# Optimization experiments

Hardware: AMD Instinct MI355X
Metric: run time of the kernel (lower is better)

The kernel has to match this reference:

```python
import jax, jax.numpy as jnp
import numpy as np

D_MODEL, N_HEAD, D_FFN = 1024, 16, 4096
MAX_REL = 128
NUM_BUCKETS = 2 * MAX_REL - 1  # 255
B, T = 2, 2048


def algebraic_ln(x, gamma, beta, a, b_raw, eps=1e-5):
    mean = jnp.mean(x, axis=-1, keepdims=True)
    var = jnp.var(x, axis=-1, keepdims=True)  # unbiased=False
    z = var + eps
    b = jax.nn.softplus(10.0 * b_raw) / 10.0  # softplus with beta=10
    p = a[0] + a[1] * z + a[2] * z ** 2
    q = b[0] + b[1] * z + b[2] * z ** 2
    return (x - mean) * (p / q) * gamma + beta


def setup_inputs() -> dict:
    key = jax.random.key(0)
    ks = jax.random.split(key, 16)
    s = (1.0 / np.sqrt(D_MODEL)).astype(np.float32)
    inp = {
        'x': jax.random.normal(ks[0], (B, T, D_MODEL), jnp.float32),
        'casual_mask': jnp.tril(jnp.ones((T, T), dtype=bool)),
        'Wq': jax.random.normal(ks[1], (D_MODEL, D_MODEL), jnp.float32) * s,
        'bq': jnp.zeros((D_MODEL,), jnp.float32),
        'Wk': jax.random.normal(ks[2], (D_MODEL, D_MODEL), jnp.float32) * s,
        'bk': jnp.zeros((D_MODEL,), jnp.float32),
        'Wv': jax.random.normal(ks[3], (D_MODEL, D_MODEL), jnp.float32) * s,
        'bv': jnp.zeros((D_MODEL,), jnp.float32),
        'Wo': jax.random.normal(ks[4], (D_MODEL, D_MODEL), jnp.float32) * s,
        'bo': jnp.zeros((D_MODEL,), jnp.float32),
        'rel_emb': jax.random.normal(ks[5], (NUM_BUCKETS, N_HEAD), jnp.float32) * 0.02,
        'g1': jnp.ones((D_MODEL,), jnp.float32),
        'be1': jnp.zeros((D_MODEL,), jnp.float32),
        'a1': jnp.array([1.0, 0.5, 0.1], jnp.float32),
        'br1': jnp.array([1.0, 0.3, 0.05], jnp.float32),
        'g2': jnp.ones((D_MODEL,), jnp.float32),
        'be2': jnp.zeros((D_MODEL,), jnp.float32),
        'a2': jnp.array([1.0, 0.5, 0.1], jnp.float32),
        'br2': jnp.array([1.0, 0.3, 0.05], jnp.float32),
        'W1': jax.random.normal(ks[6], (D_FFN, D_MODEL), jnp.float32) * s,
        'b1': jnp.zeros((D_FFN,), jnp.float32),
        'W2': jax.random.normal(ks[7], (D_MODEL, D_FFN), jnp.float32) * (1.0 / np.sqrt(D_FFN)),
        'b2': jnp.zeros((D_MODEL,), jnp.float32),
        'res_scale': jnp.array(0.5, jnp.float32),
    }
    return inp


def attention(x, mask, Wq, bq, Wk, bk, Wv, bv, Wo, bo, rel_emb):
    Bx, Tx, C = x.shape
    H, Dh = N_HEAD, C // N_HEAD
    scale = Dh ** -0.5
    Q = (x @ Wq.T + bq).reshape(Bx, Tx, H, Dh)
    K = (x @ Wk.T + bk).reshape(Bx, Tx, H, Dh)
    V = (x @ Wv.T + bv).reshape(Bx, Tx, H, Dh)
    scores = jnp.einsum('bqhd,bkhd->bhqk', Q, K) * scale
    rel = jnp.arange(Tx)[None, :] - jnp.arange(Tx)[:, None]  # k_pos - q_pos
    buckets = jnp.clip(rel, -MAX_REL + 1, MAX_REL - 1) + (MAX_REL - 1)
    bias = rel_emb[buckets]  # [T,T,H]
    scores = scores + jnp.transpose(bias, (2, 0, 1))[None]
    m = mask[None, None]  # [1,1,T,T]
    # torch: masked_fill(-inf) then masked_fill(0) -> masked entries become 0
    scores = jnp.where(m, scores, 0.0)
    w = jax.nn.relu(scores) + 1e-6
    w = jnp.where(m, w, 0.0)
    w = w / (jnp.sum(w, axis=-1, keepdims=True) + 1e-6)
    out = jnp.einsum('bhqk,bkhd->bqhd', w, V).reshape(Bx, Tx, C)
    return out @ Wo.T + bo


def reference(x, casual_mask, Wq, bq, Wk, bk, Wv, bv, Wo, bo, rel_emb,
              g1, be1, a1, br1, g2, be2, a2, br2, W1, b1, W2, b2, res_scale):
    scale = jnp.clip(res_scale, 0.2, 1.0)
    x = x + scale * attention(algebraic_ln(x, g1, be1, a1, br1), casual_mask,
                              Wq, bq, Wk, bk, Wv, bv, Wo, bo, rel_emb)
    h = algebraic_ln(x, g2, be2, a2, br2)
    ffn = jax.nn.relu(h @ W1.T + b1) @ W2.T + b2  # dropout is identity at eval
    return x + scale * ffn
```

## Files before the change

kernel.cpp:

```cpp
#include <hip/hip_runtime.h>
#include <stdint.h>


#define D_MODEL 1024
#define T_SEQ   2048
#define NHEAD   16
#define DH      64
#define DFFN    4096
#define MROWS   4096

using short8  = __attribute__((ext_vector_type(8))) short;
using floatx4 = __attribute__((ext_vector_type(4))) float;

__device__ __forceinline__ float bf2f(ushort u) {
    union { uint32_t i; float f; } x; x.i = ((uint32_t)u) << 16; return x.f;
}
__device__ __forceinline__ ushort f2bf(float f) {
    union { float f; uint32_t i; } x; x.f = f;
    uint32_t i = x.i;
    return (ushort)((i + 0x7fffu + ((i >> 16) & 1u)) >> 16);
}
__device__ __forceinline__ float ldf(const void* p, size_t i, int dt) {
    return dt ? bf2f(((const ushort*)p)[i]) : ((const float*)p)[i];
}
__device__ __forceinline__ int detect_bf16(const void* g1) {
    return *(const uint32_t*)g1 == 0x3F803F80u;
}
__device__ __forceinline__ void gld_lds16(const void* g, void* l) {
    __builtin_amdgcn_global_load_lds(
        (__attribute__((address_space(1))) uint32_t*)(g),
        (__attribute__((address_space(3))) uint32_t*)(l), 16, 0, 0);
}
__device__ __forceinline__ float softplus10(float t) {
    float u = 10.f * t;
    return (u > 20.f ? u : log1pf(expf(u))) * 0.1f;
}

template <int INMODE>
__global__ __launch_bounds__(256)
void ln_kernel(const void* __restrict__ xin,
               const void* __restrict__ gamma, const void* __restrict__ beta,
               const void* __restrict__ a3, const void* __restrict__ br3,
               ushort* __restrict__ out, const void* __restrict__ dtprobe)
{
    const int dt = detect_bf16(dtprobe);
    const int row = blockIdx.x;
    const int tid = threadIdx.x;
    const int col = tid * 4;
    float v[4];
    if (INMODE == 1) {
        const float* x = (const float*)xin + (size_t)row * D_MODEL;
        float4 t = *(const float4*)(x + col);
        v[0] = t.x; v[1] = t.y; v[2] = t.z; v[3] = t.w;
    } else if (dt) {
        const ushort* x = (const ushort*)xin + (size_t)row * D_MODEL;
        ushort4 t = *(const ushort4*)(x + col);
        v[0] = bf2f(t.x); v[1] = bf2f(t.y); v[2] = bf2f(t.z); v[3] = bf2f(t.w);
    } else {
        const float* x = (const float*)xin + (size_t)row * D_MODEL;
        float4 t = *(const float4*)(x + col);
        v[0] = t.x; v[1] = t.y; v[2] = t.z; v[3] = t.w;
    }
    float s  = v[0] + v[1] + v[2] + v[3];
    float s2 = v[0]*v[0] + v[1]*v[1] + v[2]*v[2] + v[3]*v[3];
#pragma unroll
    for (int m = 32; m > 0; m >>= 1) {
        s  += __shfl_down(s,  m, 64);
        s2 += __shfl_down(s2, m, 64);
    }
    __shared__ float wsum[4], wsum2[4];
    const int wave = tid >> 6, lane = tid & 63;
    if (lane == 0) { wsum[wave] = s; wsum2[wave] = s2; }
    __syncthreads();
    s  = wsum[0] + wsum[1] + wsum[2] + wsum[3];
    s2 = wsum2[0] + wsum2[1] + wsum2[2] + wsum2[3];
    const float mean = s * (1.f / D_MODEL);
    const float var  = s2 * (1.f / D_MODEL) - mean * mean;
    const float z = var + 1e-5f;
    const float a0 = ldf(a3, 0, dt), a1 = ldf(a3, 1, dt), a2 = ldf(a3, 2, dt);
    const float b0 = softplus10(ldf(br3, 0, dt));
    const float b1 = softplus10(ldf(br3, 1, dt));
    const float b2 = softplus10(ldf(br3, 2, dt));
    const float p = a0 + a1 * z + a2 * z * z;
    const float q = b0 + b1 * z + b2 * z * z;
    const float f = p / q;
    ushort4 o; ushort* op = (ushort*)&o;
#pragma unroll
    for (int e = 0; e < 4; e++) {
        op[e] = f2bf((v[e] - mean) * f * ldf(gamma, col + e, dt) + ldf(beta, col + e, dt));
    }
    *(ushort4*)(out + (size_t)row * D_MODEL + col) = o;
}

template <int MODE, int BM, int BN>
__global__ __launch_bounds__(256)
void gemm_bt(const ushort* __restrict__ A,
             const void* __restrict__ Bw0, const void* __restrict__ Bw1,
             const void* __restrict__ Bw2,
             const void* __restrict__ bias0, const void* __restrict__ bias1,
             const void* __restrict__ bias2,
             void* __restrict__ C0, void* __restrict__ C1, void* __restrict__ C2v,
             int Nst, int K, const void* __restrict__ dtprobe)
{
    constexpr int NI = BM / 32;
    constexpr int NJ = BN / 32;
    constexpr int AC = BM / 64;
    constexpr int BC = BN / 64;
    __shared__ __align__(16) ushort As[BM * 32];
    __shared__ __align__(16) ushort Bs[BN * 32];
    const int dt = detect_bf16(dtprobe);
    const int tid  = threadIdx.x;
    const int wave = tid >> 6, lane = tid & 63;
    const int wr = wave >> 1, wc = wave & 1;
    const int g = lane >> 4, l15 = lane & 15;

    const void* Bw = Bw0; const void* bias = bias0; void* Cout = C0;
    if (MODE == 4) {
        const int mat = blockIdx.x >> 3;
        if (mat == 1)      { Bw = Bw1; bias = bias1; Cout = C1; }
        else if (mat == 2) { Bw = Bw2; bias = bias2; Cout = C2v; }
    }
    const int m0 = blockIdx.y * BM;
    const int n0 = (MODE == 4) ? ((blockIdx.x & 7) * 128) : (blockIdx.x * BN);

    floatx4 acc[NI][NJ];
#pragma unroll
    for (int i = 0; i < NI; i++)
#pragma unroll
        for (int j = 0; j < NJ; j++) acc[i][j] = {0.f, 0.f, 0.f, 0.f};

    const int srow = lane >> 2;
    const int ssw  = (srow >> 1) & 3;
    const int scol = (((lane & 3) ^ ssw) * 8);
    const int fsw  = (l15 >> 1) & 3;
    for (int k0 = 0; k0 < K; k0 += 32) {
        __syncthreads();
        if (dt) {
            const ushort* Bb = (const ushort*)Bw;
#pragma unroll
            for (int c = 0; c < AC; c++) {
                const int r0 = (wave * AC + c) * 16;
                gld_lds16(A + (size_t)(m0 + r0 + srow) * K + k0 + scol, &As[r0 * 32]);
            }
#pragma unroll
            for (int c = 0; c < BC; c++) {
                const int r0 = (wave * BC + c) * 16;
                gld_lds16(Bb + (size_t)(n0 + r0 + srow) * K + k0 + scol, &Bs[r0 * 32]);
            }
        } else {
            const float* Bf = (const float*)Bw;
#pragma unroll
            for (int c = 0; c < AC; c++) {
                const int r0 = (wave * AC + c) * 16;
                gld_lds16(A + (size_t)(m0 + r0 + srow) * K + k0 + scol, &As[r0 * 32]);
            }
#pragma unroll
            for (int c = 0; c < BC; c++) {
                const int r0 = (wave * BC + c) * 16;
                const float* src = Bf + (size_t)(n0 + r0 + srow) * K + k0 + scol;
                float4 t0 = *(const float4*)(src);
                float4 t1 = *(const float4*)(src + 4);
                ushort tmp[8] = { f2bf(t0.x), f2bf(t0.y), f2bf(t0.z), f2bf(t0.w),
                                  f2bf(t1.x), f2bf(t1.y), f2bf(t1.z), f2bf(t1.w) };
                *(short8*)&Bs[(r0 + srow) * 32 + (lane & 3) * 8] = *(short8*)tmp;
            }
        }
        __syncthreads();
        short8 af[NI], bfr[NJ];
#pragma unroll
        for (int i = 0; i < NI; i++)
            af[i]  = *(const short8*)&As[(wr * (BM / 2) + i * 16 + l15) * 32 + ((g ^ fsw) * 8)];
#pragma unroll
        for (int j = 0; j < NJ; j++)
            bfr[j] = *(const short8*)&Bs[(wc * (BN / 2) + j * 16 + l15) * 32 + ((g ^ fsw) * 8)];
#pragma unroll
        for (int i = 0; i < NI; i++)
#pragma unroll
            for (int j = 0; j < NJ; j++)
                acc[i][j] = __builtin_amdgcn_mfma_f32_16x16x32_bf16(af[i], bfr[j], acc[i][j], 0, 0, 0);
    }

#pragma unroll
    for (int i = 0; i < NI; i++) {
        const int rowb = m0 + wr * (BM / 2) + i * 16 + g * 4;
#pragma unroll
        for (int j = 0; j < NJ; j++) {
            const int col = n0 + wc * (BN / 2) + j * 16 + l15;
            const float bi = ldf(bias, col, dt);
#pragma unroll
            for (int r = 0; r < 4; r++) {
                const size_t idx = (size_t)(rowb + r) * Nst + col;
                const float v = acc[i][j][r] + bi;
                if (MODE == 1) ((ushort*)Cout)[idx] = f2bf(fmaxf(v, 0.f));
                else           ((ushort*)Cout)[idx] = f2bf(v);
            }
        }
    }
}

template <int MODE>
__global__ __launch_bounds__(256)
void gemm_k64p(const ushort* __restrict__ A, const void* __restrict__ Bw,
               const void* __restrict__ bias, void* __restrict__ Cout,
               const void* __restrict__ resid, const void* __restrict__ scale_p,
               int Nst, int K, const void* __restrict__ dtprobe)
{
    __shared__ __align__(16) ushort As[2][2][64 * 32];
    __shared__ __align__(16) ushort Bs[2][2][64 * 32];
    const int dt = detect_bf16(dtprobe);
    const int tid  = threadIdx.x;
    const int wave = tid >> 6, lane = tid & 63;
    const int wr = wave >> 1, wc = wave & 1;
    const int g = lane >> 4, l15 = lane & 15;
    const int m0 = blockIdx.y * 64, n0 = blockIdx.x * 64;

    floatx4 acc[2][2];
#pragma unroll
    for (int i = 0; i < 2; i++)
#pragma unroll
        for (int j = 0; j < 2; j++) acc[i][j] = {0.f, 0.f, 0.f, 0.f};

    const int srow = lane >> 2;
    const int ssw  = (srow >> 1) & 3;
    const int scol = (((lane & 3) ^ ssw) * 8);
    const int fsw  = (l15 >> 1) & 3;
    const int r0   = wave * 16;

    auto stage = [&](int buf, int k0) {
        if (dt) {
            const ushort* Bb = (const ushort*)Bw;
#pragma unroll
            for (int kb = 0; kb < 2; kb++) {
                gld_lds16(A  + (size_t)(m0 + r0 + srow) * K + k0 + kb * 32 + scol, &As[buf][kb][r0 * 32]);
                gld_lds16(Bb + (size_t)(n0 + r0 + srow) * K + k0 + kb * 32 + scol, &Bs[buf][kb][r0 * 32]);
            }
        } else {
            const float* Bf = (const float*)Bw;
#pragma unroll
            for (int kb = 0; kb < 2; kb++) {
                gld_lds16(A + (size_t)(m0 + r0 + srow) * K + k0 + kb * 32 + scol, &As[buf][kb][r0 * 32]);
                const float* src = Bf + (size_t)(n0 + r0 + srow) * K + k0 + kb * 32 + scol;
                float4 t0 = *(const float4*)(src);
                float4 t1 = *(const float4*)(src + 4);
                ushort tmp[8] = { f2bf(t0.x), f2bf(t0.y), f2bf(t0.z), f2bf(t0.w),
                                  f2bf(t1.x), f2bf(t1.y), f2bf(t1.z), f2bf(t1.w) };
                *(short8*)&Bs[buf][kb][(r0 + srow) * 32 + (lane & 3) * 8] = *(short8*)tmp;
            }
        }
    };

    const int nt = K >> 6;
    stage(0, 0);
    __syncthreads();
    int cur = 0;
    for (int t = 0; t < nt; ++t) {
        if (t + 1 < nt) stage(cur ^ 1, (t + 1) << 6);
        short8 af[2][2], bfr[2][2];
#pragma unroll
        for (int kb = 0; kb < 2; kb++) {
#pragma unroll
            for (int i = 0; i < 2; i++)
                af[i][kb]  = *(const short8*)&As[cur][kb][(wr * 32 + i * 16 + l15) * 32 + ((g ^ fsw) * 8)];
#pragma unroll
            for (int j = 0; j < 2; j++)
                bfr[j][kb] = *(const short8*)&Bs[cur][kb][(wc * 32 + j * 16 + l15) * 32 + ((g ^ fsw) * 8)];
        }
#pragma unroll
        for (int kb = 0; kb < 2; kb++)
#pragma unroll
            for (int i = 0; i < 2; i++)
#pragma unroll
                for (int j = 0; j < 2; j++)
                    acc[i][j] = __builtin_amdgcn_mfma_f32_16x16x32_bf16(af[i][kb], bfr[j][kb], acc[i][j], 0, 0, 0);
        __syncthreads();
        cur ^= 1;
    }

    const float scl = fminf(fmaxf(ldf(scale_p, 0, dt), 0.2f), 1.0f);
#pragma unroll
    for (int i = 0; i < 2; i++) {
        const int rowb = m0 + wr * 32 + i * 16 + g * 4;
#pragma unroll
        for (int j = 0; j < 2; j++) {
            const int col = n0 + wc * 32 + j * 16 + l15;
            const float bi = ldf(bias, col, dt);
#pragma unroll
            for (int r = 0; r < 4; r++) {
                const size_t idx = (size_t)(rowb + r) * Nst + col;
                const float v = acc[i][j][r] + bi;
                if (MODE == 2) ((float*)Cout)[idx] = ldf(resid, idx, dt) + scl * v;
                else {
                    const float o = ((const float*)resid)[idx] + scl * v;
                    if (dt) ((ushort*)Cout)[idx] = f2bf(o);
                    else    ((float*)Cout)[idx]  = o;
                }
            }
        }
    }
}

__global__ __launch_bounds__(256)
void attn_kernel(const ushort* __restrict__ Q, const ushort* __restrict__ K,
                 const ushort* __restrict__ V, const void* __restrict__ rel,
                 ushort* __restrict__ Out, const void* __restrict__ dtprobe)
{
    __shared__ __align__(16) ushort Ks[64 * 64];
    __shared__ __align__(16) ushort Vt[64 * 88];
    __shared__ __align__(16) ushort Ss[64 * 88];
    __shared__ float rel_h[128];
    __shared__ float den_l[64];

    const int dt = detect_bf16(dtprobe);
    const int tid  = threadIdx.x;
    const int wave = tid >> 6, lane = tid & 63;
    const int wr = wave >> 1, wc = wave & 1;
    const int g = lane >> 4, l15 = lane & 15;
    const int pair = blockIdx.x, h = blockIdx.y, b = blockIdx.z;

    if (tid < 128) rel_h[tid] = ldf(rel, (size_t)tid * NHEAD + h, dt);
    const float scale = 0.125f;

    for (int ph = 0; ph < 2; ph++) {
        const int qt = ph ? (31 - pair) : pair;
        __syncthreads();
        if (tid < 64) den_l[tid] = 0.f;

        const ushort* Qg = Q + ((size_t)(b * T_SEQ + qt * 64)) * D_MODEL + h * DH;
        short8 qa[2][2];
#pragma unroll
        for (int i = 0; i < 2; i++)
#pragma unroll
            for (int ks = 0; ks < 2; ks++)
                qa[i][ks] = *(const short8*)(Qg + (size_t)(wr * 32 + i * 16 + l15) * D_MODEL
                                             + (ks * 4 + g) * 8);

        floatx4 onum[2][2];
#pragma unroll
        for (int i = 0; i < 2; i++) { onum[i][0] = {0.f,0.f,0.f,0.f}; onum[i][1] = {0.f,0.f,0.f,0.f}; }
        float den_p[2][4];
#pragma unroll
        for (int i = 0; i < 2; i++)
#pragma unroll
            for (int r = 0; r < 4; r++) den_p[i][r] = 0.f;

        const int nk = qt + 1;
        for (int kt = 0; kt < nk; kt++) {
            const int kbase = kt * 64;
            __syncthreads();
            const ushort* Kg = K + ((size_t)(b * T_SEQ + kbase)) * D_MODEL + h * DH;
            {
                const int lrow = lane >> 3, pch = lane & 7;
#pragma unroll
                for (int c = 0; c < 2; c++) {
                    const int r0 = (wave * 2 + c) * 8;
                    const int row = r0 + lrow;
                    gld_lds16(Kg + (size_t)row * D_MODEL + ((pch ^ (row & 7)) * 8), &Ks[r0 * 64]);
                }
            }
            const ushort* Vg = V + ((size_t)(b * T_SEQ + kbase)) * D_MODEL + h * DH;
#pragma unroll
            for (int c = 0; c < 2; c++) {
                const int chunk = tid + c * 256;
                const int krow = chunk >> 3;
                const int bb   = chunk & 7;
                short8 t = *(const short8*)(Vg + (size_t)krow * D_MODEL + bb * 8);
                ushort tmp[8]; *(short8*)tmp = t;
#pragma unroll
                for (int e = 0; e < 8; e++) {
                    const int ee = (e + bb) & 7;
                    Vt[(bb * 8 + ee) * 88 + krow] = tmp[ee];
                }
            }
            __syncthreads();

            floatx4 sacc[2][2];
#pragma unroll
            for (int i = 0; i < 2; i++) { sacc[i][0] = {0.f,0.f,0.f,0.f}; sacc[i][1] = {0.f,0.f,0.f,0.f}; }
#pragma unroll
            for (int ks = 0; ks < 2; ks++) {
                short8 kb[2];
                const int ch = ks * 4 + g;
#pragma unroll
                for (int j = 0; j < 2; j++) {
                    const int row = wc * 32 + j * 16 + l15;
                    kb[j] = *(const short8*)&Ks[row * 64 + ((ch ^ (row & 7)) * 8)];
                }
#pragma unroll
                for (int i = 0; i < 2; i++)
#pragma unroll
                    for (int j = 0; j < 2; j++)
                        sacc[i][j] = __builtin_amdgcn_mfma_f32_16x16x32_bf16(qa[i][ks], kb[j], sacc[i][j], 0, 0, 0);
            }

            const int dq = qt - kt;
            if (dq >= 3) {
                const float c0 = rel_h[0];
#pragma unroll
                for (int i = 0; i < 2; i++) {
                    const int qrow = wr * 32 + i * 16 + g * 4;
#pragma unroll
                    for (int j = 0; j < 2; j++) {
                        const int kcol = wc * 32 + j * 16 + l15;
#pragma unroll
                        for (int r = 0; r < 4; r++) {
                            const float w = fmaxf(sacc[i][j][r] * scale + c0, 0.f) + 1e-6f;
                            den_p[i][r] += w;
                            Ss[(qrow + r) * 88 + kcol] = f2bf(w);
                        }
                    }
                }
            } else {
#pragma unroll
                for (int i = 0; i < 2; i++) {
                    const int qrow = wr * 32 + i * 16 + g * 4;
#pragma unroll
                    for (int j = 0; j < 2; j++) {
                        const int kcol = wc * 32 + j * 16 + l15;
                        const int kg = kbase + kcol;
#pragma unroll
                        for (int r = 0; r < 4; r++) {
                            const int qg = qt * 64 + qrow + r;
                            const int d = qg - kg;
                            float w = 0.f;
                            if (d >= 0) {
                                const int bucket = 127 - (d < 127 ? d : 127);
                                const float sv = sacc[i][j][r] * scale + rel_h[bucket];
                                w = fmaxf(sv, 0.f) + 1e-6f;
                            }
                            den_p[i][r] += w;
                            Ss[(qrow + r) * 88 + kcol] = f2bf(w);
                        }
                    }
                }
            }
            __syncthreads();

#pragma unroll
            for (int ks = 0; ks < 2; ks++) {
                short8 wa[2], vb[2];
#pragma unroll
                for (int i = 0; i < 2; i++)
                    wa[i] = *(const short8*)&Ss[(wr * 32 + i * 16 + l15) * 88 + ks * 32 + g * 8];
#pragma unroll
                for (int j = 0; j < 2; j++)
                    vb[j] = *(const short8*)&Vt[(wc * 32 + j * 16 + l15) * 88 + ks * 32 + g * 8];
#pragma unroll
                for (int i = 0; i < 2; i++)
#pragma unroll
                    for (int j = 0; j < 2; j++)
                        onum[i][j] = __builtin_amdgcn_mfma_f32_16x16x32_bf16(wa[i], vb[j], onum[i][j], 0, 0, 0);
            }
        }

#pragma unroll
        for (int i = 0; i < 2; i++)
#pragma unroll
            for (int r = 0; r < 4; r++) {
                float v = den_p[i][r];
                v += __shfl_xor(v, 1, 64);
                v += __shfl_xor(v, 2, 64);
                v += __shfl_xor(v, 4, 64);
                v += __shfl_xor(v, 8, 64);
                den_p[i][r] = v;
            }
        __syncthreads();
        if (l15 == 0) {
#pragma unroll
            for (int i = 0; i < 2; i++)
#pragma unroll
                for (int r = 0; r < 4; r++)
                    atomicAdd(&den_l[wr * 32 + i * 16 + g * 4 + r], den_p[i][r]);
        }
        __syncthreads();

        const size_t obase = ((size_t)(b * T_SEQ + qt * 64)) * D_MODEL + h * DH;
#pragma unroll
        for (int i = 0; i < 2; i++) {
            const int qrow = wr * 32 + i * 16 + g * 4;
#pragma unroll
            for (int j = 0; j < 2; j++) {
                const int dcol = wc * 32 + j * 16 + l15;
#pragma unroll
                for (int r = 0; r < 4; r++) {
                    const float dn = den_l[qrow + r] + 1e-6f;
                    Out[obase + (size_t)(qrow + r) * D_MODEL + dcol] = f2bf(onum[i][j][r] / dn);
                }
            }
        }
    }
}

extern "C" void kernel_launch(void* const* d_in, const int* in_sizes, int n_in,
                              void* d_out, int out_size, void* d_ws, size_t ws_size,
                              hipStream_t stream)
{
    const void* x   = d_in[0];
    const void* Wq  = d_in[2];
    const void* bq  = d_in[3];
    const void* Wk  = d_in[4];
    const void* bk  = d_in[5];
    const void* Wv  = d_in[6];
    const void* bv  = d_in[7];
    const void* Wo  = d_in[8];
    const void* bo  = d_in[9];
    const void* rel = d_in[10];
    const void* g1  = d_in[11];
    const void* be1 = d_in[12];
    const void* a1  = d_in[13];
    const void* br1 = d_in[14];
    const void* g2  = d_in[15];
    const void* be2 = d_in[16];
    const void* a2  = d_in[17];
    const void* br2 = d_in[18];
    const void* W1  = d_in[19];
    const void* b1  = d_in[20];
    const void* W2  = d_in[21];
    const void* b2  = d_in[22];
    const void* rs  = d_in[23];

    char* ws = (char*)d_ws;
    ushort* ln1  = (ushort*)(ws);
    ushort* Qb   = (ushort*)(ws + (8u  << 20));
    ushort* Kb   = (ushort*)(ws + (16u << 20));
    ushort* Vb   = (ushort*)(ws + (24u << 20));
    ushort* atb  = (ushort*)(ws + (32u << 20));
    float*  x1   = (float*)(ws + (40u << 20));
    ushort* hbuf = (ushort*)(ws + (56u << 20));
    ushort* ffn1 = (ushort*)(ws);

    const dim3 blk(256);

    ln_kernel<0><<<dim3(MROWS), blk, 0, stream>>>(x, g1, be1, a1, br1, ln1, g1);
    gemm_bt<4, 128, 128><<<dim3(24, MROWS / 128), blk, 0, stream>>>(
        ln1, Wq, Wk, Wv, bq, bk, bv, Qb, Kb, Vb, D_MODEL, D_MODEL, g1);
    attn_kernel<<<dim3(16, NHEAD, 2), blk, 0, stream>>>(Qb, Kb, Vb, rel, atb, g1);
    gemm_k64p<2><<<dim3(D_MODEL / 64, MROWS / 64), blk, 0, stream>>>(
        atb, Wo, bo, x1, x, rs, D_MODEL, D_MODEL, g1);
    ln_kernel<1><<<dim3(MROWS), blk, 0, stream>>>(x1, g2, be2, a2, br2, hbuf, g1);
    gemm_bt<1, 128, 128><<<dim3(DFFN / 128, MROWS / 128), blk, 0, stream>>>(
        hbuf, W1, nullptr, nullptr, b1, nullptr, nullptr, ffn1, nullptr, nullptr,
        DFFN, D_MODEL, g1);
    gemm_k64p<3><<<dim3(D_MODEL / 64, MROWS / 64), blk, 0, stream>>>(
        ffn1, W2, b2, d_out, x1, rs, D_MODEL, DFFN, g1);
}
```

Baseline: 505.8 us.

## Split-K the FFN down-projection with atomic accumulation into the residual buffer

The final W2 GEMM (K=4096) is replaced by a split-K kernel over two K halves. Each half atomically adds its scaled partial sums into x1, which the second LN kernel has already pre-loaded with the residual plus scaled b2 bias. A separate cast kernel then writes the output in the input dtype. This doubles the number of blocks for the long-K GEMM to improve occupancy, at the cost of float atomics, non-deterministic summation order, and an extra pass over the output.

```diff
diff --git a/kernel.cpp b/kernel.cpp
--- a/kernel.cpp
+++ b/kernel.cpp
@@ -41,14 +41,15 @@
 void ln_kernel(const void* __restrict__ xin,
                const void* __restrict__ gamma, const void* __restrict__ beta,
                const void* __restrict__ a3, const void* __restrict__ br3,
-               ushort* __restrict__ out, const void* __restrict__ dtprobe)
+               ushort* __restrict__ out, const void* __restrict__ dtprobe,
+               const void* __restrict__ b2fold, const void* __restrict__ scale_p)
 {
     const int dt = detect_bf16(dtprobe);
     const int row = blockIdx.x;
     const int tid = threadIdx.x;
     const int col = tid * 4;
     float v[4];
-    if (INMODE == 1) {
+    if (INMODE >= 1) {
         const float* x = (const float*)xin + (size_t)row * D_MODEL;
         float4 t = *(const float4*)(x + col);
         v[0] = t.x; v[1] = t.y; v[2] = t.z; v[3] = t.w;
@@ -90,6 +91,33 @@
         op[e] = f2bf((v[e] - mean) * f * ldf(gamma, col + e, dt) + ldf(beta, col + e, dt));
     }
     *(ushort4*)(out + (size_t)row * D_MODEL + col) = o;
+    if (INMODE == 2) {
+        const float scl = fminf(fmaxf(ldf(scale_p, 0, dt), 0.2f), 1.0f);
+        float* xw = (float*)xin + (size_t)row * D_MODEL;
+        float4 t;
+        t.x = v[0] + scl * ldf(b2fold, col + 0, dt);
+        t.y = v[1] + scl * ldf(b2fold, col + 1, dt);
+        t.z = v[2] + scl * ldf(b2fold, col + 2, dt);
+        t.w = v[3] + scl * ldf(b2fold, col + 3, dt);
+        *(float4*)(xw + col) = t;
+    }
+}
+
+__global__ __launch_bounds__(256)
+void cast_out(const float* __restrict__ x1, void* __restrict__ out,
+              const void* __restrict__ dtprobe)
+{
+    const int dt = detect_bf16(dtprobe);
+    const int row = blockIdx.x;
+    const int col = threadIdx.x * 4;
+    float4 t = *(const float4*)(x1 + (size_t)row * D_MODEL + col);
+    if (dt) {
+        ushort4 o;
+        o.x = f2bf(t.x); o.y = f2bf(t.y); o.z = f2bf(t.z); o.w = f2bf(t.w);
+        *(ushort4*)((ushort*)out + (size_t)row * D_MODEL + col) = o;
+    } else {
+        *(float4*)((float*)out + (size_t)row * D_MODEL + col) = t;
+    }
 }
 
 template <int MODE, int BM, int BN>
@@ -294,6 +322,91 @@
                     if (dt) ((ushort*)Cout)[idx] = f2bf(o);
                     else    ((float*)Cout)[idx]  = o;
                 }
+            }
+        }
+    }
+}
+
+__global__ __launch_bounds__(256)
+void gemm_k64s(const ushort* __restrict__ A, const void* __restrict__ Bw,
+               float* __restrict__ Cacc, const void* __restrict__ scale_p,
+               int Nst, int K, int kext, const void* __restrict__ dtprobe)
+{
+    __shared__ __align__(16) ushort As[2][64 * 32];
+    __shared__ __align__(16) ushort Bs[2][64 * 32];
+    const int dt = detect_bf16(dtprobe);
+    const int tid  = threadIdx.x;
+    const int wave = tid >> 6, lane = tid & 63;
+    const int wr = wave >> 1, wc = wave & 1;
+    const int g = lane >> 4, l15 = lane & 15;
+    const int m0 = blockIdx.y * 64, n0 = blockIdx.x * 64;
+    const int ks0 = blockIdx.z * kext;
+
+    floatx4 acc[2][2];
+#pragma unroll
+    for (int i = 0; i < 2; i++)
+#pragma unroll
+        for (int j = 0; j < 2; j++) acc[i][j] = {0.f, 0.f, 0.f, 0.f};
+
+    const int srow = lane >> 2;
+    const int ssw  = (srow >> 1) & 3;
+    const int scol = (((lane & 3) ^ ssw) * 8);
+    const int fsw  = (l15 >> 1) & 3;
+    const int r0   = wave * 16;
+
+    for (int k0 = ks0; k0 < ks0 + kext; k0 += 64) {
+        __syncthreads();
+        if (dt) {
+            const ushort* Bb = (const ushort*)Bw;
+#pragma unroll
+            for (int kb = 0; kb < 2; kb++) {
+                gld_lds16(A  + (size_t)(m0 + r0 + srow) * K + k0 + kb * 32 + scol, &As[kb][r0 * 32]);
+                gld_lds16(Bb + (size_t)(n0 + r0 + srow) * K + k0 + kb * 32 + scol, &Bs[kb][r0 * 32]);
+            }
+        } else {
+            const float* Bf = (const float*)Bw;
+#pragma unroll
+            for (int kb = 0; kb < 2; kb++) {
+                gld_lds16(A + (size_t)(m0 + r0 + srow) * K + k0 + kb * 32 + scol, &As[kb][r0 * 32]);
+                const float* src = Bf + (size_t)(n0 + r0 + srow) * K + k0 + kb * 32 + scol;
+                float4 t0 = *(const float4*)(src);
+                float4 t1 = *(const float4*)(src + 4);
+                ushort tmp[8] = { f2bf(t0.x), f2bf(t0.y), f2bf(t0.z), f2bf(t0.w),
+                                  f2bf(t1.x), f2bf(t1.y), f2bf(t1.z), f2bf(t1.w) };
+                *(short8*)&Bs[kb][(r0 + srow) * 32 + (lane & 3) * 8] = *(short8*)tmp;
+            }
+        }
+        __syncthreads();
+        short8 af[2][2], bfr[2][2];
+#pragma unroll
+        for (int kb = 0; kb < 2; kb++) {
+#pragma unroll
+            for (int i = 0; i < 2; i++)
+                af[i][kb]  = *(const short8*)&As[kb][(wr * 32 + i * 16 + l15) * 32 + ((g ^ fsw) * 8)];
+#pragma unroll
+            for (int j = 0; j < 2; j++)
+                bfr[j][kb] = *(const short8*)&Bs[kb][(wc * 32 + j * 16 + l15) * 32 + ((g ^ fsw) * 8)];
+        }
+#pragma unroll
+        for (int kb = 0; kb < 2; kb++)
+#pragma unroll
+            for (int i = 0; i < 2; i++)
+#pragma unroll
+                for (int j = 0; j < 2; j++)
+                    acc[i][j] = __builtin_amdgcn_mfma_f32_16x16x32_bf16(af[i][kb], bfr[j][kb], acc[i][j], 0, 0, 0);
+    }
+
+    const float scl = fminf(fmaxf(ldf(scale_p, 0, dt), 0.2f), 1.0f);
+#pragma unroll
+    for (int i = 0; i < 2; i++) {
+        const int rowb = m0 + wr * 32 + i * 16 + g * 4;
+#pragma unroll
+        for (int j = 0; j < 2; j++) {
+            const int col = n0 + wc * 32 + j * 16 + l15;
+#pragma unroll
+            for (int r = 0; r < 4; r++) {
+                const size_t idx = (size_t)(rowb + r) * Nst + col;
+                atomicAdd(&Cacc[idx], scl * acc[i][j][r]);
             }
         }
     }
@@ -530,16 +643,19 @@
 
     const dim3 blk(256);
 
-    ln_kernel<0><<<dim3(MROWS), blk, 0, stream>>>(x, g1, be1, a1, br1, ln1, g1);
+    ln_kernel<0><<<dim3(MROWS), blk, 0, stream>>>(x, g1, be1, a1, br1, ln1, g1,
+                                                  nullptr, nullptr);
     gemm_bt<4, 128, 128><<<dim3(24, MROWS / 128), blk, 0, stream>>>(
         ln1, Wq, Wk, Wv, bq, bk, bv, Qb, Kb, Vb, D_MODEL, D_MODEL, g1);
     attn_kernel<<<dim3(16, NHEAD, 2), blk, 0, stream>>>(Qb, Kb, Vb, rel, atb, g1);
     gemm_k64p<2><<<dim3(D_MODEL / 64, MROWS / 64), blk, 0, stream>>>(
         atb, Wo, bo, x1, x, rs, D_MODEL, D_MODEL, g1);
-    ln_kernel<1><<<dim3(MROWS), blk, 0, stream>>>(x1, g2, be2, a2, br2, hbuf, g1);
+    ln_kernel<2><<<dim3(MROWS), blk, 0, stream>>>(x1, g2, be2, a2, br2, hbuf, g1,
+                                                  b2, rs);
     gemm_bt<1, 128, 128><<<dim3(DFFN / 128, MROWS / 128), blk, 0, stream>>>(
         hbuf, W1, nullptr, nullptr, b1, nullptr, nullptr, ffn1, nullptr, nullptr,
         DFFN, D_MODEL, g1);
-    gemm_k64p<3><<<dim3(D_MODEL / 64, MROWS / 64), blk, 0, stream>>>(
-        ffn1, W2, b2, d_out, x1, rs, D_MODEL, DFFN, g1);
-}
+    gemm_k64s<<<dim3(D_MODEL / 64, MROWS / 64, 2), blk, 0, stream>>>(
+        ffn1, W2, x1, rs, D_MODEL, DFFN, DFFN / 2, g1);
+    cast_out<<<dim3(MROWS), blk, 0, stream>>>(x1, d_out, g1);
+}
```

After: 507.5 us. No clear change (+0.3%).
